# Kernel tuning notes

Hardware: AMD Instinct MI355X
Metric: run time of the kernel (lower is better)

Reference implementation:

```python
import jax, jax.numpy as jnp
import numpy as np

B, C, H, W = 2, 72, 96, 96
FACTOR = 4  # input_dim // output_dim = 72 // 18


def setup_inputs() -> dict:
    key = jax.random.key(0)
    ks = jax.random.split(key, 7)
    s = 1.0 / np.sqrt(C)
    return {
        "x": jax.random.normal(ks[0], (B, C, H, W), dtype=jnp.float32),
        "Wq": jax.random.normal(ks[1], (C, C), dtype=jnp.float32) * s,
        "bq": jax.random.normal(ks[2], (C,), dtype=jnp.float32) * 0.01,
        "Wk": jax.random.normal(ks[3], (C, C), dtype=jnp.float32) * s,
        "bk": jax.random.normal(ks[4], (C,), dtype=jnp.float32) * 0.01,
        "Wv": jax.random.normal(ks[5], (C, C), dtype=jnp.float32) * s,
        "bv": jax.random.normal(ks[6], (C,), dtype=jnp.float32) * 0.01,
    }


def reference(x, Wq, bq, Wk, bk, Wv, bv):
    b, c, h, w = x.shape
    n = h * w
    flat = x.reshape(b, c, n)  # [B, C, N]
    # 1x1 convs == per-pixel channel matmuls
    q = jnp.einsum('dc,bcn->bdn', Wq, flat) + bq[None, :, None]
    k = jnp.einsum('dc,bcn->bdn', Wk, flat) + bk[None, :, None]
    v = jnp.einsum('dc,bcn->bdn', Wv, flat) + bv[None, :, None]
    # scores[b,i,j] = sum_c q[b,c,i] * k[b,c,j]  (no 1/sqrt(d) scaling, as in source)
    scores = jnp.einsum('bci,bcj->bij', q, k)  # [B, N, N]
    attn = jax.nn.softmax(scores, axis=-1)
    # weighted_values = bmm(v, attn^T): wv[b,c,i] = sum_j v[b,c,j] * attn[b,i,j]
    wv = jnp.einsum('bcj,bij->bci', v, attn)  # [B, C, N]
    wv = wv.reshape(b, c // FACTOR, FACTOR, h, w)
    xg = x.reshape(b, c // FACTOR, FACTOR, h, w)
    pooled = jnp.sum(xg * wv, axis=2)  # [B, C//FACTOR, H, W]
    return pooled
```

## Files before the change

### kernel.cpp

```cpp
#include <hip/hip_runtime.h>

#define NPIX 9216
#define CIN 72
#define CP 96
#define SPLITS 8
#define JCHUNK (NPIX / SPLITS)
#define JTILES (JCHUNK / 64)
#define L2E   1.44269504088896f
#define EXPB  46.1662413084468f

typedef __attribute__((ext_vector_type(8))) short bf16x8;
typedef __attribute__((ext_vector_type(8))) _Float16 f16x8;
typedef __attribute__((ext_vector_type(4))) float f32x4;

#define MFMA_BF16(A,B,C) __builtin_amdgcn_mfma_f32_16x16x32_bf16(A,B,C,0,0,0)
#define MFMA_F16(A,B,C)  __builtin_amdgcn_mfma_f32_16x16x32_f16(A,B,C,0,0,0)

static __device__ __forceinline__ unsigned short f2bf(float f) {
  unsigned u = __float_as_uint(f);
  u += 0x7fffu + ((u >> 16) & 1u);
  return (unsigned short)(u >> 16);
}
static __device__ __forceinline__ float bf2f(unsigned short h) {
  return __uint_as_float(((unsigned)h) << 16);
}
static __device__ __forceinline__ unsigned short f2h(float f) {
  _Float16 h = (_Float16)f;
  return *(unsigned short*)&h;
}
static __device__ __forceinline__ unsigned pack_bf_trunc(float lo, float hi) {
  return (__float_as_uint(lo) >> 16) | (__float_as_uint(hi) & 0xffff0000u);
}
static __device__ __forceinline__ void load_lds16(const void* g, void* l) {
  __builtin_amdgcn_global_load_lds(
      (const __attribute__((address_space(1))) unsigned int*)g,
      (__attribute__((address_space(3))) unsigned int*)l, 16, 0, 0);
}

__global__ __launch_bounds__(256) void wprep_kernel(
    const float* __restrict__ Wq, const float* __restrict__ Wk,
    const float* __restrict__ Wv,
    unsigned short* __restrict__ WH, unsigned short* __restrict__ WL)
{
  int id = blockIdx.x * 256 + threadIdx.x;
  if (id >= 3 * 80 * 96) return;
  int mat = id / (80 * 96);
  int rem = id % (80 * 96);
  int d = rem / 96, c = rem % 96;
  const float* W = (mat == 0) ? Wq : (mat == 1) ? Wk : Wv;
  float v = (d < 72 && c < 72) ? W[d * 72 + c] : 0.f;
  unsigned short hi = f2bf(v);
  WH[id] = hi;
  WL[id] = f2bf(v - bf2f(hi));
}

#define XTS 104
#define QS  4

static __device__ __forceinline__ void stage_x(const float* __restrict__ x,
    float* lbuf, int b, int n0, int w, int lane) {
#pragma unroll
  for (int kk = 0; kk < 2; ++kk) {
    const int ch = w * 2 + kk;
    const int r = ch * 16 + (lane >> 2);
    const int c = (r < 72) ? r : 71;
    const float* src = x + ((size_t)b * CIN + c) * NPIX + n0 + (lane & 3) * 4;
    load_lds16(src, lbuf + ch * 256);
  }
}

__global__ __launch_bounds__(192, 1) void qkv_kernel(
    const float* __restrict__ x,
    const unsigned short* __restrict__ WH, const unsigned short* __restrict__ WL,
    const float* __restrict__ bq, const float* __restrict__ bk,
    const float* __restrict__ bv,
    unsigned short* __restrict__ QH, unsigned short* __restrict__ KH,
    unsigned short* __restrict__ VG)
{
  __shared__ __align__(16) float ls_x[2][6 * 256];
  __shared__ __align__(16) unsigned short obuf[2][16 * XTS];

  const int t    = threadIdx.x;
  const int w    = t >> 6;
  const int lane = t & 63;
  const int quad = lane >> 4;
  const int l15  = lane & 15;
  const int bid  = blockIdx.x;
  const int b    = bid / 144;
  const int g0   = bid % 144;
  const int nbase = g0 * 64;

  const unsigned short* wh = WH + w * 80 * 96;
  const unsigned short* wl = WL + w * 80 * 96;
  bf16x8 WAh[5][3], WAl[5][3];
#pragma unroll
  for (int dm = 0; dm < 5; ++dm)
#pragma unroll
    for (int ks = 0; ks < 3; ++ks) {
      WAh[dm][ks] = *(const bf16x8*)(wh + (dm * 16 + l15) * 96 + ks * 32 + quad * 8);
      WAl[dm][ks] = *(const bf16x8*)(wl + (dm * 16 + l15) * 96 + ks * 32 + quad * 8);
    }
  const float* bias = (w == 0) ? bq : (w == 1) ? bk : bv;
  float bs[5][4];
#pragma unroll
  for (int dm = 0; dm < 5; ++dm)
#pragma unroll
    for (int r = 0; r < 4; ++r) {
      int d = dm * 16 + quad * 4 + r;
      bs[dm][r] = (d < 72) ? bias[d] : 0.f;
    }

  stage_x(x, ls_x[0], b, nbase, w, lane);
  __syncthreads();

  for (int s = 0; s < QS; ++s) {
    const int n0 = nbase + s * 16;
    if (s + 1 < QS) stage_x(x, ls_x[(s + 1) & 1], b, n0 + 16, w, lane);
    const float* lx = ls_x[s & 1];

    bf16x8 xbh[3], xbl[3];
#pragma unroll
    for (int ks = 0; ks < 3; ++ks) {
#pragma unroll
      for (int j = 0; j < 8; ++j) {
        float v = lx[(ks * 32 + quad * 8 + j) * 16 + l15];
        unsigned short hi = f2bf(v);
        ((unsigned short*)&xbh[ks])[j] = hi;
        ((unsigned short*)&xbl[ks])[j] = f2bf(v - bf2f(hi));
      }
    }

    f32x4 acc[5];
#pragma unroll
    for (int dm = 0; dm < 5; ++dm) {
      acc[dm] = (f32x4){0.f, 0.f, 0.f, 0.f};
#pragma unroll
      for (int ks = 0; ks < 3; ++ks) {
        acc[dm] = MFMA_BF16(WAh[dm][ks], xbh[ks], acc[dm]);
        acc[dm] = MFMA_BF16(WAh[dm][ks], xbl[ks], acc[dm]);
        acc[dm] = MFMA_BF16(WAl[dm][ks], xbh[ks], acc[dm]);
      }
    }

    if (w < 2) {
      unsigned short* ob = obuf[w];
#pragma unroll
      for (int dm = 0; dm < 5; ++dm)
#pragma unroll
        for (int r = 0; r < 4; ++r) {
          int d = dm * 16 + quad * 4 + r;
          float v = acc[dm][r] + bs[dm][r];
          ob[l15 * XTS + d] = f2h(v);
        }
      unsigned short* outp = (w == 0) ? QH : KH;
      const size_t obase = ((size_t)b * NPIX + n0) * CP;
      uint4 z; z.x = z.y = z.z = z.w = 0u;
      for (int f = lane; f < 192; f += 64) {
        int row = f / 12, col = f % 12;
        *(uint4*)(outp + obase + (size_t)row * CP + col * 8) =
            (col < 10) ? *(const uint4*)(ob + row * XTS + col * 8) : z;
      }
    } else {
#pragma unroll
      for (int dm = 0; dm < 5; ++dm)
#pragma unroll
        for (int r = 0; r < 4; ++r) {
          int d = dm * 16 + quad * 4 + r;
          float v = (d < 72) ? acc[dm][r] + bs[dm][r] : (d == 72 ? 1.0f : 0.f);
          VG[((size_t)b * 80 + d) * NPIX + n0 + l15] = f2bf(v);
        }
    }
    __syncthreads();
  }
}

#define KCH 12
#define VCH 10

__global__ __launch_bounds__(256, 3) void flash_kernel(
    const float* __restrict__ x,
    const unsigned short* __restrict__ QH, const unsigned short* __restrict__ KH,
    const unsigned short* __restrict__ VG,
    float* __restrict__ NUM, float* __restrict__ LPART)
{
  __shared__ __align__(16) unsigned short ls_kh[KCH * 512];
  __shared__ __align__(16) unsigned short ls_vs[VCH * 512];

  const int t    = threadIdx.x;
  const int w    = t >> 6;
  const int lane = t & 63;
  const int quad = lane >> 4;
  const int l15  = lane & 15;

  const int bid  = blockIdx.x;
  const int sp   = bid & 7;
  const int slot = bid >> 3;
  const int b    = slot / 48;
  const int it   = slot % 48;
  const int i0w  = it * 192 + w * 48;

  f16x8 qh[3][3];
#pragma unroll
  for (int mi = 0; mi < 3; ++mi)
#pragma unroll
    for (int ks = 0; ks < 3; ++ks) {
      size_t off = ((size_t)b * NPIX + i0w + mi * 16 + l15) * CP + ks * 32 + quad * 8;
      qh[mi][ks] = *(const f16x8*)(QH + off);
    }

  f32x4 oacc[3][5];
#pragma unroll
  for (int mi = 0; mi < 3; ++mi)
#pragma unroll
    for (int nt = 0; nt < 5; ++nt) oacc[mi][nt] = (f32x4){0.f, 0.f, 0.f, 0.f};

  const unsigned short* kpg = KH + ((size_t)b * NPIX + sp * JCHUNK) * CP;
  const unsigned short* vpg = VG + (size_t)b * 80 * NPIX + sp * JCHUNK;

  int koff[3], voff[3];
#pragma unroll
  for (int k = 0; k < 3; ++k) {
    int c = w + 4 * k;
    koff[k] = ((c / 3) * 16 + l15) * CP + (c % 3) * 32 + quad * 8;
    int cv = (c < VCH) ? c : 0;
    voff[k] = ((cv >> 1) * 16 + l15) * NPIX + (cv & 1) * 32 + quad * 8;
  }

  for (int jt = 0; jt < JTILES; ++jt, kpg += 64 * CP, vpg += 64) {
#pragma unroll
    for (int k = 0; k < 3; ++k)
      load_lds16(kpg + koff[k], ls_kh + (w + 4 * k) * 512);
#pragma unroll
    for (int k = 0; k < 3; ++k)
      if (w + 4 * k < VCH)
        load_lds16(vpg + voff[k], ls_vs + (w + 4 * k) * 512);
    __syncthreads();

#pragma unroll
    for (int js = 0; js < 2; ++js) {
      uint2 pkA[3], pkB[3];
#pragma unroll
      for (int tjh = 0; tjh < 2; ++tjh) {
        const int tj = js * 2 + tjh;
        f16x8 fkh[3];
#pragma unroll
        for (int ks = 0; ks < 3; ++ks)
          fkh[ks] = *(const f16x8*)(ls_kh + (tj * 3 + ks) * 512 + lane * 8);
#pragma unroll
        for (int mi = 0; mi < 3; ++mi) {
          f32x4 s = (f32x4){0.f, 0.f, 0.f, 0.f};
          s = MFMA_F16(fkh[0], qh[mi][0], s);
          s = MFMA_F16(fkh[1], qh[mi][1], s);
          s = MFMA_F16(fkh[2], qh[mi][2], s);
          float p0 = __builtin_amdgcn_exp2f(__builtin_fmaf(s[0], L2E, -EXPB));
          float p1 = __builtin_amdgcn_exp2f(__builtin_fmaf(s[1], L2E, -EXPB));
          float p2 = __builtin_amdgcn_exp2f(__builtin_fmaf(s[2], L2E, -EXPB));
          float p3 = __builtin_amdgcn_exp2f(__builtin_fmaf(s[3], L2E, -EXPB));
          uint2 pk;
          pk.x = pack_bf_trunc(p0, p1);
          pk.y = pack_bf_trunc(p2, p3);
          if (tjh == 0) pkA[mi] = pk; else pkB[mi] = pk;
        }
      }

      bf16x8 pf[3];
#pragma unroll
      for (int mi = 0; mi < 3; ++mi) {
        unsigned x0 = pkA[mi].x, x1 = pkB[mi].x;
        asm("v_permlane32_swap_b32 %0, %1" : "+v"(x0), "+v"(x1));
        asm("v_permlane16_swap_b32 %0, %1" : "+v"(x0), "+v"(x1));
        unsigned y0 = pkA[mi].y, y1 = pkB[mi].y;
        asm("v_permlane32_swap_b32 %0, %1" : "+v"(y0), "+v"(y1));
        asm("v_permlane16_swap_b32 %0, %1" : "+v"(y0), "+v"(y1));
        uint4 fr;
        fr.x = x0; fr.y = y0; fr.z = x1; fr.w = y1;
        pf[mi] = *(const bf16x8*)&fr;
      }

#pragma unroll
      for (int nt = 0; nt < 5; ++nt) {
        bf16x8 vf = *(const bf16x8*)(ls_vs + (nt * 2 + js) * 512 + lane * 8);
#pragma unroll
        for (int mi = 0; mi < 3; ++mi)
          oacc[mi][nt] = MFMA_BF16(vf, pf[mi], oacc[mi][nt]);
      }
    }
    __syncthreads();
  }

  const size_t sb = (size_t)(sp * 2 + b);
#pragma unroll
  for (int mi = 0; mi < 3; ++mi) {
    const int i = i0w + mi * 16 + l15;
    if (quad == 2)
      LPART[sb * NPIX + i] = oacc[mi][4][0];
#pragma unroll
    for (int nt = 0; nt < 5; ++nt) {
      int c0 = nt * 16 + quad * 4;
      if (c0 < 72) {
        float num = 0.f;
#pragma unroll
        for (int r = 0; r < 4; ++r)
          num = __builtin_fmaf(x[((size_t)b * CIN + c0 + r) * NPIX + i],
                               oacc[mi][nt][r], num);
        NUM[(sb * 18 + (c0 >> 2)) * NPIX + i] = num;
      }
    }
  }
}

__global__ __launch_bounds__(256) void combine_pool_kernel(
    const float* __restrict__ NUM, const float* __restrict__ LPART,
    float* __restrict__ out)
{
  int id = blockIdx.x * 256 + threadIdx.x;
  if (id >= 2 * 18 * (NPIX / 4)) return;
  int n = (id % (NPIX / 4)) * 4;
  int rest = id / (NPIX / 4);
  int g = rest % 18, b = rest / 18;

  float4 A = make_float4(0.f, 0.f, 0.f, 0.f);
  float4 L = make_float4(0.f, 0.f, 0.f, 0.f);
#pragma unroll
  for (int s = 0; s < SPLITS; ++s) {
    size_t sb = (size_t)(s * 2 + b);
    float4 a = *(const float4*)(NUM + (sb * 18 + g) * NPIX + n);
    float4 l = *(const float4*)(LPART + sb * NPIX + n);
    A.x += a.x; A.y += a.y; A.z += a.z; A.w += a.w;
    L.x += l.x; L.y += l.y; L.z += l.z; L.w += l.w;
  }
  float4 r;
  r.x = A.x / L.x; r.y = A.y / L.y; r.z = A.z / L.z; r.w = A.w / L.w;
  *(float4*)(out + (size_t)id * 4) = r;
}

extern "C" void kernel_launch(void* const* d_in, const int* in_sizes, int n_in,
                              void* d_out, int out_size, void* d_ws, size_t ws_size,
                              hipStream_t stream) {
  const float* x  = (const float*)d_in[0];
  const float* Wq = (const float*)d_in[1];
  const float* bq = (const float*)d_in[2];
  const float* Wk = (const float*)d_in[3];
  const float* bk = (const float*)d_in[4];
  const float* Wv = (const float*)d_in[5];
  const float* bv = (const float*)d_in[6];
  float* out = (float*)d_out;

  char* p = (char*)d_ws;
  const size_t szQK = (size_t)2 * NPIX * CP * 2;
  unsigned short* QH = (unsigned short*)p; p += szQK;
  unsigned short* KH = (unsigned short*)p; p += szQK;
  unsigned short* VG = (unsigned short*)p; p += (size_t)2 * 80 * NPIX * 2;
  unsigned short* WH = (unsigned short*)p; p += (size_t)3 * 80 * 96 * 2;
  unsigned short* WL = (unsigned short*)p; p += (size_t)3 * 80 * 96 * 2;
  float* NUM = (float*)p; p += (size_t)SPLITS * 2 * 18 * NPIX * 4;
  float* LPART = (float*)p; p += (size_t)SPLITS * 2 * NPIX * 4;

  wprep_kernel<<<(3 * 80 * 96 + 255) / 256, 256, 0, stream>>>(Wq, Wk, Wv, WH, WL);
  qkv_kernel<<<288, 192, 0, stream>>>(x, WH, WL, bq, bk, bv, QH, KH, VG);
  flash_kernel<<<SPLITS * 2 * 48, 256, 0, stream>>>(x, QH, KH, VG, NUM, LPART);
  combine_pool_kernel<<<(2 * 18 * (NPIX / 4) + 255) / 256, 256, 0, stream>>>(
      NUM, LPART, out);
}
```

Measured before the change: 148.3 us.

## Split QKV projection into one wave per (strip, matrix) task across more blocks

The QKV projection kernel is restructured so that each wave handles a single 16-pixel strip for one of the Q/K/V matrices. Previously each 3-wave block kept its weights in registers and looped over four strips, with double-buffered LDS staging of x. The new version launches 864 blocks of 256 threads, reads x directly from global memory, and reloads weights per MFMA from cache. The aim is more parallelism and occupancy and no per-strip block barriers, at the cost of reading x three times (once per matrix) and reloading the weights in every wave.

```diff
diff --git a/kernel.cpp b/kernel.cpp
--- a/kernel.cpp
+++ b/kernel.cpp
@@ -55,21 +55,8 @@
 }
 
 #define XTS 104
-#define QS  4
-
-static __device__ __forceinline__ void stage_x(const float* __restrict__ x,
-    float* lbuf, int b, int n0, int w, int lane) {
-#pragma unroll
-  for (int kk = 0; kk < 2; ++kk) {
-    const int ch = w * 2 + kk;
-    const int r = ch * 16 + (lane >> 2);
-    const int c = (r < 72) ? r : 71;
-    const float* src = x + ((size_t)b * CIN + c) * NPIX + n0 + (lane & 3) * 4;
-    load_lds16(src, lbuf + ch * 256);
-  }
-}
-
-__global__ __launch_bounds__(192, 1) void qkv_kernel(
+
+__global__ __launch_bounds__(256) void qkv_kernel(
     const float* __restrict__ x,
     const unsigned short* __restrict__ WH, const unsigned short* __restrict__ WL,
     const float* __restrict__ bq, const float* __restrict__ bk,
@@ -77,100 +64,79 @@
     unsigned short* __restrict__ QH, unsigned short* __restrict__ KH,
     unsigned short* __restrict__ VG)
 {
-  __shared__ __align__(16) float ls_x[2][6 * 256];
-  __shared__ __align__(16) unsigned short obuf[2][16 * XTS];
+  __shared__ __align__(16) unsigned short obuf[4][16 * XTS];
 
   const int t    = threadIdx.x;
-  const int w    = t >> 6;
+  const int ww   = t >> 6;
   const int lane = t & 63;
   const int quad = lane >> 4;
   const int l15  = lane & 15;
-  const int bid  = blockIdx.x;
-  const int b    = bid / 144;
-  const int g0   = bid % 144;
-  const int nbase = g0 * 64;
-
-  const unsigned short* wh = WH + w * 80 * 96;
-  const unsigned short* wl = WL + w * 80 * 96;
-  bf16x8 WAh[5][3], WAl[5][3];
-#pragma unroll
-  for (int dm = 0; dm < 5; ++dm)
+
+  const int task  = blockIdx.x * 4 + ww;
+  const int m     = task % 3;
+  const int strip = task / 3;
+  const int b     = strip / 576;
+  const int n0    = (strip % 576) * 16;
+
+  bf16x8 xbh[3], xbl[3];
+#pragma unroll
+  for (int ks = 0; ks < 3; ++ks) {
+#pragma unroll
+    for (int j = 0; j < 8; ++j) {
+      int c = ks * 32 + quad * 8 + j;
+      c = (c < 72) ? c : 71;
+      float v = x[((size_t)b * CIN + c) * NPIX + n0 + l15];
+      unsigned short hi = f2bf(v);
+      ((unsigned short*)&xbh[ks])[j] = hi;
+      ((unsigned short*)&xbl[ks])[j] = f2bf(v - bf2f(hi));
+    }
+  }
+
+  const unsigned short* wh = WH + m * 80 * 96;
+  const unsigned short* wl = WL + m * 80 * 96;
+  const float* bias = (m == 0) ? bq : (m == 1) ? bk : bv;
+
+  f32x4 acc[5];
+#pragma unroll
+  for (int dm = 0; dm < 5; ++dm) {
+    acc[dm] = (f32x4){0.f, 0.f, 0.f, 0.f};
 #pragma unroll
     for (int ks = 0; ks < 3; ++ks) {
-      WAh[dm][ks] = *(const bf16x8*)(wh + (dm * 16 + l15) * 96 + ks * 32 + quad * 8);
-      WAl[dm][ks] = *(const bf16x8*)(wl + (dm * 16 + l15) * 96 + ks * 32 + quad * 8);
-    }
-  const float* bias = (w == 0) ? bq : (w == 1) ? bk : bv;
-  float bs[5][4];
-#pragma unroll
-  for (int dm = 0; dm < 5; ++dm)
-#pragma unroll
-    for (int r = 0; r < 4; ++r) {
-      int d = dm * 16 + quad * 4 + r;
-      bs[dm][r] = (d < 72) ? bias[d] : 0.f;
-    }
-
-  stage_x(x, ls_x[0], b, nbase, w, lane);
-  __syncthreads();
-
-  for (int s = 0; s < QS; ++s) {
-    const int n0 = nbase + s * 16;
-    if (s + 1 < QS) stage_x(x, ls_x[(s + 1) & 1], b, n0 + 16, w, lane);
-    const float* lx = ls_x[s & 1];
-
-    bf16x8 xbh[3], xbl[3];
-#pragma unroll
-    for (int ks = 0; ks < 3; ++ks) {
-#pragma unroll
-      for (int j = 0; j < 8; ++j) {
-        float v = lx[(ks * 32 + quad * 8 + j) * 16 + l15];
-        unsigned short hi = f2bf(v);
-        ((unsigned short*)&xbh[ks])[j] = hi;
-        ((unsigned short*)&xbl[ks])[j] = f2bf(v - bf2f(hi));
-      }
-    }
-
-    f32x4 acc[5];
-#pragma unroll
-    for (int dm = 0; dm < 5; ++dm) {
-      acc[dm] = (f32x4){0.f, 0.f, 0.f, 0.f};
-#pragma unroll
-      for (int ks = 0; ks < 3; ++ks) {
-        acc[dm] = MFMA_BF16(WAh[dm][ks], xbh[ks], acc[dm]);
-        acc[dm] = MFMA_BF16(WAh[dm][ks], xbl[ks], acc[dm]);
-        acc[dm] = MFMA_BF16(WAl[dm][ks], xbh[ks], acc[dm]);
-      }
-    }
-
-    if (w < 2) {
-      unsigned short* ob = obuf[w];
-#pragma unroll
-      for (int dm = 0; dm < 5; ++dm)
-#pragma unroll
-        for (int r = 0; r < 4; ++r) {
-          int d = dm * 16 + quad * 4 + r;
-          float v = acc[dm][r] + bs[dm][r];
-          ob[l15 * XTS + d] = f2h(v);
-        }
-      unsigned short* outp = (w == 0) ? QH : KH;
-      const size_t obase = ((size_t)b * NPIX + n0) * CP;
-      uint4 z; z.x = z.y = z.z = z.w = 0u;
-      for (int f = lane; f < 192; f += 64) {
-        int row = f / 12, col = f % 12;
-        *(uint4*)(outp + obase + (size_t)row * CP + col * 8) =
-            (col < 10) ? *(const uint4*)(ob + row * XTS + col * 8) : z;
-      }
-    } else {
-#pragma unroll
-      for (int dm = 0; dm < 5; ++dm)
-#pragma unroll
-        for (int r = 0; r < 4; ++r) {
-          int d = dm * 16 + quad * 4 + r;
-          float v = (d < 72) ? acc[dm][r] + bs[dm][r] : (d == 72 ? 1.0f : 0.f);
-          VG[((size_t)b * 80 + d) * NPIX + n0 + l15] = f2bf(v);
-        }
-    }
-    __syncthreads();
+      bf16x8 ah = *(const bf16x8*)(wh + (dm * 16 + l15) * 96 + ks * 32 + quad * 8);
+      bf16x8 al = *(const bf16x8*)(wl + (dm * 16 + l15) * 96 + ks * 32 + quad * 8);
+      acc[dm] = MFMA_BF16(ah, xbh[ks], acc[dm]);
+      acc[dm] = MFMA_BF16(ah, xbl[ks], acc[dm]);
+      acc[dm] = MFMA_BF16(al, xbh[ks], acc[dm]);
+    }
+  }
+
+  if (m < 2) {
+    unsigned short* ob = obuf[ww];
+#pragma unroll
+    for (int dm = 0; dm < 5; ++dm)
+#pragma unroll
+      for (int r = 0; r < 4; ++r) {
+        int d = dm * 16 + quad * 4 + r;
+        float v = acc[dm][r] + (d < 72 ? bias[d] : 0.f);
+        ob[l15 * XTS + d] = f2h(v);
+      }
+    unsigned short* outp = (m == 0) ? QH : KH;
+    const size_t obase = ((size_t)b * NPIX + n0) * CP;
+    uint4 z; z.x = z.y = z.z = z.w = 0u;
+    for (int f = lane; f < 192; f += 64) {
+      int row = f / 12, col = f % 12;
+      *(uint4*)(outp + obase + (size_t)row * CP + col * 8) =
+          (col < 10) ? *(const uint4*)(ob + row * XTS + col * 8) : z;
+    }
+  } else {
+#pragma unroll
+    for (int dm = 0; dm < 5; ++dm)
+#pragma unroll
+      for (int r = 0; r < 4; ++r) {
+        int d = dm * 16 + quad * 4 + r;
+        float v = (d < 72) ? acc[dm][r] + bias[d] : (d == 72 ? 1.0f : 0.f);
+        VG[((size_t)b * 80 + d) * NPIX + n0 + l15] = f2bf(v);
+      }
   }
 }
 
@@ -357,7 +323,7 @@
   float* LPART = (float*)p; p += (size_t)SPLITS * 2 * NPIX * 4;
 
   wprep_kernel<<<(3 * 80 * 96 + 255) / 256, 256, 0, stream>>>(Wq, Wk, Wv, WH, WL);
-  qkv_kernel<<<288, 192, 0, stream>>>(x, WH, WL, bq, bk, bv, QH, KH, VG);
+  qkv_kernel<<<864, 256, 0, stream>>>(x, WH, WL, bq, bk, bv, QH, KH, VG);
   flash_kernel<<<SPLITS * 2 * 48, 256, 0, stream>>>(x, QH, KH, VG, NUM, LPART);
   combine_pool_kernel<<<(2 * 18 * (NPIX / 4) + 255) / 256, 256, 0, stream>>>(
       NUM, LPART, out);
```

Measured after the change: 153.3 us. 3.3% more time.
